# Kernel tuning notes

Measured on AMD Instinct MI355X. Metric: run time of the kernel, lower is better.

The kernel has to match this reference:

```python
import jax, jax.numpy as jnp
import numpy as np

B, C, Hs, Ws = 8, 512, 32, 32
NUM_HEADS, D_K = 8, 64
SCALE = D_K ** -0.5


def setup_inputs() -> dict:
    key = jax.random.key(0)
    ks = jax.random.split(key, 8)
    inner = NUM_HEADS * D_K  # 512
    s = 0.02
    return {
        "x": jax.random.normal(ks[0], (B, C, Hs, Ws), dtype=jnp.float32),
        "y": jax.random.normal(ks[1], (B, C, Hs, Ws), dtype=jnp.float32),
        "Wq": jax.random.normal(ks[2], (inner, C), dtype=jnp.float32) * s,
        "bq": jnp.zeros((inner,), dtype=jnp.float32),
        "Wkv": jax.random.normal(ks[3], (2 * inner, C), dtype=jnp.float32) * s,
        "bkv": jnp.zeros((2 * inner,), dtype=jnp.float32),
        "Wp": jax.random.normal(ks[4], (C, inner), dtype=jnp.float32) * s,
        "bp": jnp.zeros((C,), dtype=jnp.float32),
    }


def reference(x, y, Wq, bq, Wkv, bkv, Wp, bp):
    # Faithful to CrossAttentionBlock.forward: y is only shape-checked, unused.
    x_shape = x.shape
    b, c = x.shape[0], x.shape[1]
    # channel_transfer: [B, C, H, W] -> [B, H, W, C] -> [B, N, C]
    xt = jnp.transpose(x, (0, 2, 3, 1)).reshape(b, -1, c)
    n = xt.shape[1]
    # q: [B, N, H*dk] -> [B, H, N, dk]
    q = (xt @ Wq.T + bq).reshape(b, n, NUM_HEADS, D_K).transpose(0, 2, 1, 3)
    # kv: [B, N, 2*H*dk] -> [2, B, H, N, dk]
    kv = (xt @ Wkv.T + bkv).reshape(b, n, 2, NUM_HEADS, D_K).transpose(2, 0, 3, 1, 4)
    k, v = kv[0], kv[1]
    atten = jnp.einsum("bhik,bhjk->bhij", q, k) * SCALE
    atten = jax.nn.softmax(atten, axis=-1)
    res = jnp.einsum("bhij,bhjd->bhid", atten, v)  # [B, H, N, dk]
    res = res.transpose(0, 2, 1, 3).reshape(b, n, NUM_HEADS * D_K)
    res = res @ Wp.T + bp  # [B, N, C]
    # original does a raw reshape of [B, N, C] back into x_shape [B, C, H, W]
    return res.reshape(x_shape)
```

## Files before the change

kernel.cpp:

```cpp
#include <hip/hip_runtime.h>
#include <math.h>

#define BB 8
#define CC 512
#define NH 8
#define DK 64
#define NN 1024
#define MROWS (BB * NN)
#define INNER 512
#define QSCALE 0.18033688011112042f


typedef __attribute__((ext_vector_type(8))) short bf16x8;
typedef __attribute__((ext_vector_type(4))) float floatx4;
typedef __attribute__((ext_vector_type(16))) float floatx16;

__device__ inline short f2bf(float f) {
    union { float f; unsigned u; } un;
    un.f = f;
    unsigned r = un.u + 0x7fffu + ((un.u >> 16) & 1u);
    return (short)(r >> 16);
}

#if defined(__has_builtin)
#if __has_builtin(__builtin_amdgcn_exp2f)
#define EXP2(x) __builtin_amdgcn_exp2f(x)
#else
#define EXP2(x) __expf((x) * 0.69314718056f)
#endif
#else
#define EXP2(x) __expf((x) * 0.69314718056f)
#endif

#define GLD_LDS(gptr, lptr)                                                  \
    __builtin_amdgcn_global_load_lds(                                        \
        (const __attribute__((address_space(1))) void*)(gptr),               \
        (__attribute__((address_space(3))) void*)(lptr), 16, 0, 0)

__global__ __launch_bounds__(256) void prep_kernel(
    const float* __restrict__ x, const float* __restrict__ Wq,
    const float* __restrict__ Wkv, const float* __restrict__ Wp,
    const float* __restrict__ bq, const float* __restrict__ bkv,
    short* __restrict__ xtb, short* __restrict__ wqkvb,
    short* __restrict__ wpb, float* __restrict__ bqkv) {
    __shared__ float tile[32][33];
    const int bid = blockIdx.x;
    if (bid < 4096) {
        const int n0 = (bid & 31) * 32;
        const int c0 = ((bid >> 5) & 15) * 32;
        const int b = bid >> 9;
        const int tx = threadIdx.x & 31;
        const int ty = threadIdx.x >> 5;
        const float* xb = x + (size_t)b * CC * NN;
        short* xo = xtb + (size_t)b * NN * CC;
        for (int i = ty; i < 32; i += 8)
            tile[i][tx] = xb[(size_t)(c0 + i) * NN + n0 + tx];
        __syncthreads();
        for (int i = ty; i < 32; i += 8)
            xo[(size_t)(n0 + i) * CC + c0 + tx] = f2bf(tile[tx][i]);
    } else {
        const int i = (bid - 4096) * 1024 + threadIdx.x * 4;
        if (i < 786432) {
            float4 v = (i < 262144) ? *(const float4*)&Wq[i]
                                    : *(const float4*)&Wkv[i - 262144];
            wqkvb[i + 0] = f2bf(v.x);
            wqkvb[i + 1] = f2bf(v.y);
            wqkvb[i + 2] = f2bf(v.z);
            wqkvb[i + 3] = f2bf(v.w);
        } else if (i < 1048576) {
            const int j = i - 786432;
            float4 v = *(const float4*)&Wp[j];
            wpb[j + 0] = f2bf(v.x);
            wpb[j + 1] = f2bf(v.y);
            wpb[j + 2] = f2bf(v.z);
            wpb[j + 3] = f2bf(v.w);
        } else {
            const int j = i - 1048576;
            if (j < 1536) {
                float4 v = (j < 512) ? *(const float4*)&bq[j]
                                     : *(const float4*)&bkv[j - 512];
                *(float4*)&bqkv[j] = v;
            }
        }
    }
}

template <int MODE, int BN>
__global__ __launch_bounds__(256) void gemm_mfma_kernel(
    const short* __restrict__ A, const short* __restrict__ W,
    const float* __restrict__ bias, float* __restrict__ outf,
    short* __restrict__ outq, short* __restrict__ outk,
    short* __restrict__ outv) {
    constexpr int K = 512;
    constexpr int WCOLS = BN / 64;
    constexpr int WROWS = 4 / WCOLS;
    constexpr int WRSPAN = 128 / WROWS;
    constexpr int RT = WRSPAN / 16;
    constexpr int ABUF = 128 * 32;
    constexpr int BBUF = BN * 32;
    constexpr int STAGE_EL = 2 * ABUF + 2 * BBUF;
    constexpr int CS_EL = (MODE == 1) ? 128 * 132 : 0;
    constexpr int SMEM_EL = (CS_EL > STAGE_EL) ? CS_EL : STAGE_EL;
    __shared__ short smem[SMEM_EL];
    short* As = smem;
    short* Bs = smem + 2 * ABUF;

    const int t = threadIdx.x;
    const int wave = t >> 6;
    const int lane = t & 63;
    const int col = lane & 15;
    const int quad = lane >> 4;
    const int wr = wave / WCOLS;
    const int wc = wave % WCOLS;

    const int bm0 = blockIdx.x * 128;
    const int bn0 = blockIdx.y * BN;

    floatx4 acc[RT][4];
#pragma unroll
    for (int i = 0; i < RT; i++)
#pragma unroll
        for (int j = 0; j < 4; j++) acc[i][j] = (floatx4){0.f, 0.f, 0.f, 0.f};

    const int kpE = (lane & 3) * 8;
    const int rA = wave * 32 + (lane >> 2);
    const short* Ag = A + (size_t)(bm0 + rA) * K + kpE;
    const int rB = wave * (BN / 4) + (lane >> 2);
    const short* Wg = W + (size_t)(bn0 + rB) * K + kpE;
    const int aOff = wave * 1024;
    const int bOff = wave * (BN / 4) * 32;

#define GSTAGE(K0, BUF)                                                       \
    do {                                                                      \
        GLD_LDS(Ag + (K0), As + (BUF)*ABUF + aOff);                           \
        GLD_LDS(Ag + 16 * K + (K0), As + (BUF)*ABUF + aOff + 512);            \
        if constexpr (BN == 128) {                                            \
            GLD_LDS(Wg + (K0), Bs + (BUF)*BBUF + bOff);                       \
            GLD_LDS(Wg + 16 * K + (K0), Bs + (BUF)*BBUF + bOff + 512);        \
        } else {                                                              \
            GLD_LDS(Wg + (K0), Bs + (BUF)*BBUF + bOff);                       \
        }                                                                     \
    } while (0)

    GSTAGE(0, 0);

#pragma unroll
    for (int it = 0; it < 16; it++) {
        const int buf = it & 1;
        __syncthreads();
        if (it < 15) GSTAGE((it + 1) * 32, buf ^ 1);

        const short* A_ = As + buf * ABUF;
        const short* B_ = Bs + buf * BBUF;
        bf16x8 aF[RT], bF[4];
#pragma unroll
        for (int rt = 0; rt < RT; rt++)
            aF[rt] =
                *(const bf16x8*)&A_[(wr * WRSPAN + rt * 16 + col) * 32 + quad * 8];
#pragma unroll
        for (int ct = 0; ct < 4; ct++)
            bF[ct] = *(const bf16x8*)&B_[(wc * 64 + ct * 16 + col) * 32 + quad * 8];
#pragma unroll
        for (int rt = 0; rt < RT; rt++)
#pragma unroll
            for (int ct = 0; ct < 4; ct++)
                acc[rt][ct] = __builtin_amdgcn_mfma_f32_16x16x32_bf16(
                    aF[rt], bF[ct], acc[rt][ct], 0, 0, 0);
    }
#undef GSTAGE

    if (MODE == 1) {
        short* Cs = smem;
        const bool isV = (bn0 >= 1024);
        const bool isQ = (bn0 < 512);
        __syncthreads();
        if (isV) {
#pragma unroll
            for (int rt = 0; rt < RT; rt++) {
#pragma unroll
                for (int ct = 0; ct < 4; ct++) {
                    const int jn_l = wc * 64 + ct * 16 + col;
                    const float bsv = bias[bn0 + jn_l];
                    const int m_l = wr * WRSPAN + rt * 16 + quad * 4;
                    short4 v4;
                    v4.x = f2bf(acc[rt][ct][0] + bsv);
                    v4.y = f2bf(acc[rt][ct][1] + bsv);
                    v4.z = f2bf(acc[rt][ct][2] + bsv);
                    v4.w = f2bf(acc[rt][ct][3] + bsv);
                    *(short4*)&Cs[jn_l * 132 + m_l] = v4;
                }
            }
        } else {
#pragma unroll
            for (int rt = 0; rt < RT; rt++) {
#pragma unroll
                for (int ct = 0; ct < 4; ct++) {
                    const int jn_l = wc * 64 + ct * 16 + col;
                    const float bsv = bias[bn0 + jn_l];
#pragma unroll
                    for (int r = 0; r < 4; r++) {
                        const int m_l = wr * WRSPAN + rt * 16 + quad * 4 + r;
                        const float val = acc[rt][ct][r] + bsv;
                        Cs[m_l * 132 + jn_l] =
                            isQ ? f2bf(val * QSCALE) : f2bf(val);
                    }
                }
            }
        }
        __syncthreads();
        const int b = bm0 >> 10;
        const int nbase = bm0 & 1023;
        if (isV) {
#pragma unroll
            for (int p = 0; p < 8; p++) {
                const int cid = p * 256 + t;
                const int jn_l = cid >> 4;
                const int m0 = (cid & 15) * 8;
                bf16x8 frag = *(const bf16x8*)&Cs[jn_l * 132 + m0];
                const int jn_g = bn0 + jn_l;
                const int h = (jn_g >> 6) & 7;
                const int d = jn_g & 63;
                *(bf16x8*)&outv[(((size_t)(b * NH + h)) * DK + d) * NN + nbase +
                                m0] = frag;
            }
        } else {
            short* dst = isQ ? outq : outk;
#pragma unroll
            for (int p = 0; p < 8; p++) {
                const int cid = p * 256 + t;
                const int m_l = cid >> 4;
                const int jn0 = (cid & 15) * 8;
                bf16x8 frag = *(const bf16x8*)&Cs[m_l * 132 + jn0];
                const int jn_g = bn0 + jn0;
                const int h = (jn_g >> 6) & 7;
                const int d = jn_g & 63;
                *(bf16x8*)&dst[(((size_t)(b * NH + h)) * NN + nbase + m_l) * DK +
                               d] = frag;
            }
        }
        return;
    }

#pragma unroll
    for (int rt = 0; rt < RT; rt++) {
#pragma unroll
        for (int ct = 0; ct < 4; ct++) {
            const int jn = bn0 + wc * 64 + ct * 16 + col;
            const float bsv = bias[jn];
#pragma unroll
            for (int r = 0; r < 4; r++) {
                const int m = bm0 + wr * WRSPAN + rt * 16 + quad * 4 + r;
                outf[(size_t)m * 512 + jn] = acc[rt][ct][r] + bsv;
            }
        }
    }
}

__global__ __launch_bounds__(256) void attn_mfma_kernel(
    const short* __restrict__ q, const short* __restrict__ k,
    const short* __restrict__ vt, short* __restrict__ out) {
    const int bh = blockIdx.x;
    const int b = bh >> 3;
    const int h = bh & 7;
    const int n0 = blockIdx.y * 128;
    const int tid = threadIdx.x;
    const int wave = tid >> 6;
    const int lane = tid & 63;
    const int l31 = lane & 31;
    const int hi = lane >> 5;
    const int rsw = l31 & 7;

    __shared__ short Ks[2][64 * 64];
    __shared__ short Vs[2][64 * 64];

    bf16x8 qf[4];
    {
        const size_t qbase =
            ((size_t)bh * NN + n0 + wave * 32 + l31) * DK + hi * 8;
#pragma unroll
        for (int dc = 0; dc < 4; dc++)
            qf[dc] = *(const bf16x8*)&q[qbase + dc * 16];
    }

    floatx16 o[2];
#pragma unroll
    for (int dt = 0; dt < 2; dt++)
#pragma unroll
        for (int i = 0; i < 16; i++) o[dt][i] = 0.f;
    float l_run = 0.f;

    const short* kg = k + (size_t)bh * NN * DK;
    const short* vg = vt + (size_t)bh * DK * NN;

    const int srow = lane >> 3;
    const int sunit = (lane & 7) ^ srow;
    const int sbase = wave * 16;

#define STAGE(J0, BUF)                                                         \
    do {                                                                       \
        GLD_LDS(kg + (size_t)((J0) + sbase + srow) * DK + sunit * 8,           \
                &Ks[BUF][sbase * 64]);                                         \
        GLD_LDS(kg + (size_t)((J0) + sbase + 8 + srow) * DK + sunit * 8,       \
                &Ks[BUF][(sbase + 8) * 64]);                                   \
        GLD_LDS(vg + (size_t)(sbase + srow) * NN + (J0) + sunit * 8,           \
                &Vs[BUF][sbase * 64]);                                         \
        GLD_LDS(vg + (size_t)(sbase + 8 + srow) * NN + (J0) + sunit * 8,       \
                &Vs[BUF][(sbase + 8) * 64]);                                   \
    } while (0)

    STAGE(0, 0);

    for (int c = 0; c < 16; c++) {
        const int buf = c & 1;
        __syncthreads();
        if (c < 15) STAGE((c + 1) * 64, buf ^ 1);

        const short* K_ = &Ks[buf][0];
        const short* V_ = &Vs[buf][0];

        floatx16 sacc[2];
#pragma unroll
        for (int kt = 0; kt < 2; kt++) {
#pragma unroll
            for (int i = 0; i < 16; i++) sacc[kt][i] = 0.f;
#pragma unroll
            for (int dc = 0; dc < 4; dc++) {
                bf16x8 kf = *(const bf16x8*)&K_[(kt * 32 + l31) * 64 +
                                                (((dc * 2 + hi) ^ rsw) * 8)];
                sacc[kt] = __builtin_amdgcn_mfma_f32_32x32x16_bf16(
                    kf, qf[dc], sacc[kt], 0, 0, 0);
            }
        }

        unsigned pw[2][4][2];
#pragma unroll
        for (int kt = 0; kt < 2; kt++) {
            float p[16];
#pragma unroll
            for (int i = 0; i < 16; i++) p[i] = EXP2(sacc[kt][i]);
            float s0 = (p[0] + p[1]) + (p[2] + p[3]);
            float s1 = (p[4] + p[5]) + (p[6] + p[7]);
            float s2 = (p[8] + p[9]) + (p[10] + p[11]);
            float s3 = (p[12] + p[13]) + (p[14] + p[15]);
            l_run += (s0 + s1) + (s2 + s3);
#pragma unroll
            for (int s = 0; s < 4; s++)
#pragma unroll
                for (int j = 0; j < 2; j++)
                    asm("v_cvt_pk_bf16_f32 %0, %1, %2"
                        : "=v"(pw[kt][s][j])
                        : "v"(p[4 * s + 2 * j]), "v"(p[4 * s + 2 * j + 1]));
#pragma unroll
            for (int cc = 0; cc < 2; cc++)
#pragma unroll
                for (int j = 0; j < 2; j++)
                    asm("v_permlane32_swap_b32 %0, %1"
                        : "+v"(pw[kt][2 * cc][j]), "+v"(pw[kt][2 * cc + 1][j]));
        }
        bf16x8 PA[4];
#pragma unroll
        for (int kc = 0; kc < 4; kc++) {
            const int kt = kc >> 1, cc = kc & 1;
            union { unsigned w[4]; bf16x8 v; } pa;
            pa.w[0] = pw[kt][2 * cc][0];
            pa.w[1] = pw[kt][2 * cc][1];
            pa.w[2] = pw[kt][2 * cc + 1][0];
            pa.w[3] = pw[kt][2 * cc + 1][1];
            PA[kc] = pa.v;
        }

#pragma unroll
        for (int dt = 0; dt < 2; dt++)
#pragma unroll
            for (int kc = 0; kc < 4; kc++) {
                bf16x8 vf = *(const bf16x8*)&V_[(dt * 32 + l31) * 64 +
                                                (((kc * 2 + hi) ^ rsw) * 8)];
                o[dt] = __builtin_amdgcn_mfma_f32_32x32x16_bf16(PA[kc], vf,
                                                                o[dt], 0, 0, 0);
            }
    }
#undef STAGE

    l_run += __shfl_xor(l_run, 32, 64);
    const float inv = 1.f / l_run;
    float invq[4][4];
#pragma unroll
    for (int s = 0; s < 4; s++)
#pragma unroll
        for (int rr = 0; rr < 4; rr++)
            invq[s][rr] = __shfl(inv, 4 * hi + rr + 8 * s, 64);

#pragma unroll
    for (int dt = 0; dt < 2; dt++)
#pragma unroll
        for (int s = 0; s < 4; s++)
#pragma unroll
            for (int rr = 0; rr < 4; rr++) {
                const int qloc = 4 * hi + rr + 8 * s;
                const int m = n0 + wave * 32 + qloc;
                out[((size_t)(b * NN + m)) * 512 + h * 64 + dt * 32 + l31] =
                    f2bf(o[dt][4 * s + rr] * invq[s][rr]);
            }
}

extern "C" void kernel_launch(void* const* d_in, const int* in_sizes, int n_in,
                              void* d_out, int out_size, void* d_ws,
                              size_t ws_size, hipStream_t stream) {
    const float* x = (const float*)d_in[0];
    const float* Wq = (const float*)d_in[2];
    const float* bq = (const float*)d_in[3];
    const float* Wkv = (const float*)d_in[4];
    const float* bkv = (const float*)d_in[5];
    const float* Wp = (const float*)d_in[6];
    const float* bp = (const float*)d_in[7];
    float* out = (float*)d_out;

    short* ws = (short*)d_ws;
    short* xtb = ws;
    short* qb = xtb + (size_t)MROWS * CC;
    short* kb = qb + (size_t)MROWS * INNER;
    short* vb = kb + (size_t)MROWS * INNER;
    short* wqkvb = vb + (size_t)MROWS * INNER;
    short* wpb = wqkvb + (size_t)3 * INNER * CC;
    float* bqkv = (float*)(wpb + (size_t)CC * INNER);
    short* att = xtb;

    prep_kernel<<<4096 + 1026, 256, 0, stream>>>(x, Wq, Wkv, Wp, bq, bkv, xtb,
                                                 wqkvb, wpb, bqkv);
    {
        dim3 grid(MROWS / 128, (3 * INNER) / 128);
        gemm_mfma_kernel<1, 128><<<grid, 256, 0, stream>>>(
            xtb, wqkvb, bqkv, nullptr, qb, kb, vb);
    }
    {
        dim3 grid(BB * NH, NN / 128);
        attn_mfma_kernel<<<grid, 256, 0, stream>>>(qb, kb, vb, att);
    }
    {
        dim3 grid(MROWS / 128, CC / 64);
        gemm_mfma_kernel<0, 64><<<grid, 256, 0, stream>>>(
            att, wpb, bp, out, nullptr, nullptr, nullptr);
    }
}
```

Measured before the change: 145.0 us.

## Deepen LDS prefetch to four buffers with explicit vmcnt waits in GEMM and attention

```diff
diff --git a/kernel.cpp b/kernel.cpp
--- a/kernel.cpp
+++ b/kernel.cpp
@@ -36,6 +36,9 @@
     __builtin_amdgcn_global_load_lds(                                        \
         (const __attribute__((address_space(1))) void*)(gptr),               \
         (__attribute__((address_space(3))) void*)(lptr), 16, 0, 0)
+
+#define BARRIER() __builtin_amdgcn_s_barrier()
+#define WAITCNT_VM(N) asm volatile("s_waitcnt vmcnt(" #N ")" ::: "memory")
 
 __global__ __launch_bounds__(256) void prep_kernel(
     const float* __restrict__ x, const float* __restrict__ Wq,
@@ -98,12 +101,11 @@
     constexpr int RT = WRSPAN / 16;
     constexpr int ABUF = 128 * 32;
     constexpr int BBUF = BN * 32;
-    constexpr int STAGE_EL = 2 * ABUF + 2 * BBUF;
+    constexpr int BUFEL = ABUF + BBUF;
+    constexpr int STAGE_EL = 4 * BUFEL;
     constexpr int CS_EL = (MODE == 1) ? 128 * 132 : 0;
     constexpr int SMEM_EL = (CS_EL > STAGE_EL) ? CS_EL : STAGE_EL;
     __shared__ short smem[SMEM_EL];
-    short* As = smem;
-    short* Bs = smem + 2 * ABUF;
 
     const int t = threadIdx.x;
     const int wave = t >> 6;
@@ -132,26 +134,33 @@
 
 #define GSTAGE(K0, BUF)                                                       \
     do {                                                                      \
-        GLD_LDS(Ag + (K0), As + (BUF)*ABUF + aOff);                           \
-        GLD_LDS(Ag + 16 * K + (K0), As + (BUF)*ABUF + aOff + 512);            \
+        short* base_ = smem + (BUF)*BUFEL;                                    \
+        GLD_LDS(Ag + (K0), base_ + aOff);                                     \
+        GLD_LDS(Ag + 16 * K + (K0), base_ + aOff + 512);                      \
         if constexpr (BN == 128) {                                            \
-            GLD_LDS(Wg + (K0), Bs + (BUF)*BBUF + bOff);                       \
-            GLD_LDS(Wg + 16 * K + (K0), Bs + (BUF)*BBUF + bOff + 512);        \
+            GLD_LDS(Wg + (K0), base_ + ABUF + bOff);                          \
+            GLD_LDS(Wg + 16 * K + (K0), base_ + ABUF + bOff + 512);           \
         } else {                                                              \
-            GLD_LDS(Wg + (K0), Bs + (BUF)*BBUF + bOff);                       \
+            GLD_LDS(Wg + (K0), base_ + ABUF + bOff);                          \
         }                                                                     \
     } while (0)
 
     GSTAGE(0, 0);
+    GSTAGE(32, 1);
 
 #pragma unroll
     for (int it = 0; it < 16; it++) {
-        const int buf = it & 1;
-        __syncthreads();
-        if (it < 15) GSTAGE((it + 1) * 32, buf ^ 1);
-
-        const short* A_ = As + buf * ABUF;
-        const short* B_ = Bs + buf * BBUF;
+        if (it < 14) {
+            GSTAGE((it + 2) * 32, (it + 2) & 3);
+            if constexpr (BN == 128) WAITCNT_VM(8);
+            else WAITCNT_VM(6);
+        } else {
+            WAITCNT_VM(0);
+        }
+        BARRIER();
+
+        const short* A_ = smem + (it & 3) * BUFEL;
+        const short* B_ = A_ + ABUF;
         bf16x8 aF[RT], bF[4];
 #pragma unroll
         for (int rt = 0; rt < RT; rt++)
@@ -270,8 +279,7 @@
     const int hi = lane >> 5;
     const int rsw = l31 & 7;
 
-    __shared__ short Ks[2][64 * 64];
-    __shared__ short Vs[2][64 * 64];
+    __shared__ short KVs[4][2 * 4096];
 
     bf16x8 qf[4];
     {
@@ -299,24 +307,29 @@
 #define STAGE(J0, BUF)                                                         \
     do {                                                                       \
         GLD_LDS(kg + (size_t)((J0) + sbase + srow) * DK + sunit * 8,           \
-                &Ks[BUF][sbase * 64]);                                         \
+                &KVs[BUF][sbase * 64]);                                        \
         GLD_LDS(kg + (size_t)((J0) + sbase + 8 + srow) * DK + sunit * 8,       \
-                &Ks[BUF][(sbase + 8) * 64]);                                   \
+                &KVs[BUF][(sbase + 8) * 64]);                                  \
         GLD_LDS(vg + (size_t)(sbase + srow) * NN + (J0) + sunit * 8,           \
-                &Vs[BUF][sbase * 64]);                                         \
+                &KVs[BUF][4096 + sbase * 64]);                                 \
         GLD_LDS(vg + (size_t)(sbase + 8 + srow) * NN + (J0) + sunit * 8,       \
-                &Vs[BUF][(sbase + 8) * 64]);                                   \
+                &KVs[BUF][4096 + (sbase + 8) * 64]);                           \
     } while (0)
 
     STAGE(0, 0);
+    STAGE(64, 1);
 
     for (int c = 0; c < 16; c++) {
-        const int buf = c & 1;
-        __syncthreads();
-        if (c < 15) STAGE((c + 1) * 64, buf ^ 1);
-
-        const short* K_ = &Ks[buf][0];
-        const short* V_ = &Vs[buf][0];
+        if (c < 14) {
+            STAGE((c + 2) * 64, (c + 2) & 3);
+            WAITCNT_VM(8);
+        } else {
+            WAITCNT_VM(0);
+        }
+        BARRIER();
+
+        const short* K_ = &KVs[c & 3][0];
+        const short* V_ = &KVs[c & 3][4096];
 
         floatx16 sacc[2];
 #pragma unroll
```

New measurement: 149.7 us. 1.03x slower.
